# Optimization experiments

Hardware: AMD Instinct MI355X
Metric: run time of the kernel (lower is better)

## Reference

```python
import jax, jax.numpy as jnp
import numpy as np

N_EMBD = 256
N_HEAD = 4
HEAD_DIM = N_EMBD // N_HEAD  # 64


def setup_inputs() -> dict:
    key = jax.random.key(0)
    k_x, k_attn, k_proj = jax.random.split(key, 3)
    B, S = 8, 2048
    x = jax.random.normal(k_x, (B, S, N_EMBD), dtype=jnp.float32)
    # nn.Linear(in, out, bias=False): weight shape [out, in]; y = x @ W.T
    std_attn = 1.0 / np.sqrt(N_EMBD)
    W_attn = jax.random.uniform(k_attn, (3 * N_EMBD, N_EMBD), dtype=jnp.float32,
                                minval=-std_attn, maxval=std_attn)
    W_proj = jax.random.uniform(k_proj, (N_EMBD, N_EMBD), dtype=jnp.float32,
                                minval=-std_attn, maxval=std_attn)
    return {"x": x, "W_attn": W_attn, "W_proj": W_proj}


def reference(x, W_attn, W_proj):
    B, S, C = x.shape
    qkv = jnp.einsum('bsc,oc->bso', x, W_attn)  # [B,S,3C]
    q, k, v = jnp.split(qkv, 3, axis=2)
    # [B,S,C] -> [B,H,S,D]
    def heads(t):
        return t.reshape(B, S, N_HEAD, HEAD_DIM).transpose(0, 2, 1, 3)
    q, k, v = heads(q), heads(k), heads(v)
    scale = 1.0 / np.sqrt(HEAD_DIM)
    scores = jnp.einsum('bhqd,bhkd->bhqk', q, k) * scale  # [B,H,S,S]
    causal = jnp.tril(jnp.ones((S, S), dtype=bool))
    scores = jnp.where(causal, scores, jnp.finfo(scores.dtype).min)
    attn = jax.nn.softmax(scores, axis=-1)
    y = jnp.einsum('bhqk,bhkd->bhqd', attn, v)  # [B,H,S,D]
    y = y.transpose(0, 2, 1, 3).reshape(B, S, C)
    return jnp.einsum('bsc,oc->bso', y, W_proj)
```

## Files before the change

kernel.cpp:

```cpp
#include <hip/hip_runtime.h>
#include <stdint.h>


#define BB 8
#define SS 2048
#define CC 256
#define HH 4
#define DD 64

typedef __attribute__((ext_vector_type(8))) __bf16 bf16x8;
typedef __attribute__((ext_vector_type(4))) __bf16 bf16x4;
typedef __attribute__((ext_vector_type(4))) float f32x4;
typedef __attribute__((ext_vector_type(16))) float f32x16;

#define CM 0.18033688011112042f

static __device__ __forceinline__ uint32_t cvtpk(float lo, float hi) {
  uint32_t r;
  asm("v_cvt_pk_bf16_f32 %0, %1, %2" : "=v"(r) : "v"(lo), "v"(hi));
  return r;
}
static __device__ __forceinline__ void pl32swap(uint32_t& a, uint32_t& b) {
  asm("v_permlane32_swap_b32 %0, %1" : "+v"(a), "+v"(b));
}
union PU { uint32_t u[4]; bf16x8 v; };

static __device__ __forceinline__ int frag_off(int row, int c8) {
  return ((row >> 4) * 8 + (c8 >> 2)) * 512 + (row & 15) * 32 + (c8 & 3) * 8;
}

__global__ __launch_bounds__(256) void cvt3_kernel(const float* __restrict__ x,
                                                   const float* __restrict__ wa,
                                                   const float* __restrict__ wp,
                                                   __bf16* __restrict__ xf,
                                                   __bf16* __restrict__ waf,
                                                   __bf16* __restrict__ wpf) {
  int i = blockIdx.x * blockDim.x + threadIdx.x;
  const float* in; __bf16* out;
  if (i < 524288) {
    in = x + i * 8;
    out = xf + frag_off(i >> 5, i & 31);
  } else if (i < 548864) {
    int j = i - 524288;
    in = wa + j * 8;
    out = waf + frag_off(j >> 5, j & 31);
  } else {
    int k = i - 548864;
    in = wp + k * 8;
    out = wpf + frag_off(k >> 5, k & 31);
  }
  float4 v0 = ((const float4*)in)[0];
  float4 v1 = ((const float4*)in)[1];
  bf16x8 o = { (__bf16)v0.x, (__bf16)v0.y, (__bf16)v0.z, (__bf16)v0.w,
               (__bf16)v1.x, (__bf16)v1.y, (__bf16)v1.z, (__bf16)v1.w };
  *(bf16x8*)out = o;
}

__global__ __launch_bounds__(256) void qkv_gemm(const __bf16* __restrict__ xf,
                                                const __bf16* __restrict__ waf,
                                                __bf16* __restrict__ qf_,
                                                __bf16* __restrict__ kf_,
                                                __bf16* __restrict__ vf_) {
  const int lane = threadIdx.x & 63;
  const int ln = lane & 15, kg = lane >> 4;
  const int w = threadIdx.x >> 6;
  const int xs = blockIdx.x & 7;
  const int j = blockIdx.x >> 3;
  const int otile = j % 12;
  const int rt0 = (xs * 8 + j / 12) * 16 + w * 4;
  const int ot0 = otile * 4;
  const int loff = ln * 32 + kg * 8;
  const bool vmode = (otile >= 8);

  f32x4 acc[4][4] = {};
  for (int cb = 0; cb < 8; ++cb) {
    bf16x8 a[4], wv[4];
#pragma unroll
    for (int i = 0; i < 4; ++i)
      a[i] = *(const bf16x8*)(xf + ((rt0 + i) * 8 + cb) * 512 + loff);
#pragma unroll
    for (int t = 0; t < 4; ++t)
      wv[t] = *(const bf16x8*)(waf + ((ot0 + t) * 8 + cb) * 512 + loff);
    if (vmode) {
#pragma unroll
      for (int i = 0; i < 4; ++i)
#pragma unroll
        for (int t = 0; t < 4; ++t)
          acc[i][t] = __builtin_amdgcn_mfma_f32_16x16x32_bf16(a[i], wv[t], acc[i][t], 0, 0, 0);
    } else {
#pragma unroll
      for (int i = 0; i < 4; ++i)
#pragma unroll
        for (int t = 0; t < 4; ++t)
          acc[i][t] = __builtin_amdgcn_mfma_f32_16x16x32_bf16(wv[t], a[i], acc[i][t], 0, 0, 0);
    }
  }
  const int r0 = rt0 * 16;
  const int o0 = ot0 * 16;
  if (!vmode) {
    const bool isK = (otile >= 4);
    const float sc = isK ? CM : 1.0f;
#pragma unroll
    for (int i = 0; i < 4; ++i) {
      int s = r0 + i * 16 + ln;
      int b = s >> 11, srow = s & 2047;
#pragma unroll
      for (int t = 0; t < 4; ++t) {
        int obase = o0 + t * 16 + kg * 4;
        int oo = obase & 255;
        int h = oo >> 6;
        int bh_off = (b * HH + h) * 131072;
        uint32_t lo = cvtpk(acc[i][t][0] * sc, acc[i][t][1] * sc);
        uint32_t hi2 = cvtpk(acc[i][t][2] * sc, acc[i][t][3] * sc);
        uint2 st = { lo, hi2 };
        if (!isK) {
          int off = bh_off + (srow >> 5) * 2048 + t * 512 + (srow & 31) * 16 + kg * 4;
          *(uint2*)(qf_ + off) = st;
        } else {
          int off = bh_off + (srow >> 6) * 4096 + t * 1024 + (srow & 63) * 16 + kg * 4;
          *(uint2*)(kf_ + off) = st;
        }
      }
    }
  } else {
    const int h = otile - 8;
#pragma unroll
    for (int i = 0; i < 4; ++i) {
      int sg = r0 + i * 16;
      int b = sg >> 11;
      int bh_off = (b * HH + h) * 131072;
      int sbase = (sg & 2047) + kg * 4;
      int off0 = bh_off + (sbase >> 6) * 4096 + ((sbase >> 4) & 3) * 1024 + (sbase & 15);
#pragma unroll
      for (int t = 0; t < 4; ++t) {
        int d = t * 16 + ln;
        uint32_t lo = cvtpk(acc[i][t][0], acc[i][t][1]);
        uint32_t hi2 = cvtpk(acc[i][t][2], acc[i][t][3]);
        uint2 st = { lo, hi2 };
        *(uint2*)(vf_ + off0 + d * 16) = st;
      }
    }
  }
}

__global__ __launch_bounds__(256, 4) void attn_kernel(const __bf16* __restrict__ qf_,
                                                      const __bf16* __restrict__ kf_,
                                                      const __bf16* __restrict__ vf_,
                                                      __bf16* __restrict__ yf) {
  __shared__ float lsum[2][32];
  __shared__ float lacc[2][64][33];
  const int lane = threadIdx.x & 63;
  const int l31 = lane & 31;
  const int hi = lane >> 5;
  const int w = threadIdx.x >> 6;
  const int kh = w & 1;
  const int cp = w >> 1;

  const int bid = blockIdx.x;
  const int xs = bid & 7;
  const int j = bid >> 3;
  const int bh = xs + 8 * (j & 3);
  const int p = j >> 2;
  const int c = (31 - p) * 2 + cp;
  const int q0w = c * 32;

  const int loff = l31 * 16 + hi * 8;
  const int koff = kh * 32;

  const __bf16* Qfb = qf_ + bh * 131072 + c * 2048 + loff;
  const __bf16* Kb  = kf_ + bh * 131072 + loff + kh * 512;
  const __bf16* Vb  = vf_ + bh * 131072 + loff + kh * 2048;

  bf16x8 qf[4];
#pragma unroll
  for (int s = 0; s < 4; ++s) qf[s] = *(const bf16x8*)(Qfb + s * 512);

  const int ntot = (q0w + 95) >> 6;
  const int qrel = l31 + 32 * (c & 1);

  f32x16 acc0 = {}, acc1 = {};
  float lrun = 0.0f;

  for (int kt = 0; kt < ntot; ++kt) {
    bf16x8 ka[4], vfr[2][2];
    {
      const __bf16* Kp = Kb + kt * 4096;
      const __bf16* Vp = Vb + kt * 4096;
#pragma unroll
      for (int s = 0; s < 4; ++s) ka[s] = *(const bf16x8*)(Kp + s * 1024);
      vfr[0][0] = *(const bf16x8*)(Vp);
      vfr[0][1] = *(const bf16x8*)(Vp + 512);
      vfr[1][0] = *(const bf16x8*)(Vp + 1024);
      vfr[1][1] = *(const bf16x8*)(Vp + 1536);
    }

    f32x16 s0 = {};
    __builtin_amdgcn_s_setprio(1);
#pragma unroll
    for (int s = 0; s < 4; ++s) s0 = __builtin_amdgcn_mfma_f32_32x32x16_bf16(ka[s], qf[s], s0, 0, 0, 0);
    __builtin_amdgcn_s_setprio(0);

    if (kt == ntot - 1) {
#pragma unroll
      for (int r = 0; r < 16; ++r) {
        int crow = (r & 3) + 8 * (r >> 2) + 4 * hi;
        s0[r] = (crow + koff <= qrel) ? s0[r] : -1e30f;
      }
    }

#pragma unroll
    for (int r = 0; r < 16; ++r) s0[r] = __builtin_amdgcn_exp2f(s0[r]);

    {
      float sm[8];
#pragma unroll
      for (int r = 0; r < 8; ++r) sm[r] = s0[r] + s0[r + 8];
#pragma unroll
      for (int st = 4; st > 0; st >>= 1)
#pragma unroll
        for (int r = 0; r < 4; ++r) if (r < st) sm[r] += sm[r + st];
      lrun += sm[0];
    }

    bf16x8 pf[2];
#pragma unroll
    for (int g = 0; g < 2; ++g) {
      const int o = g * 8;
      uint32_t a = cvtpk(s0[o + 0], s0[o + 1]);
      uint32_t b = cvtpk(s0[o + 4], s0[o + 5]);
      uint32_t c2 = cvtpk(s0[o + 2], s0[o + 3]);
      uint32_t d2 = cvtpk(s0[o + 6], s0[o + 7]);
      pl32swap(a, b);
      pl32swap(c2, d2);
      PU u; u.u[0] = a; u.u[1] = c2; u.u[2] = b; u.u[3] = d2;
      pf[g] = u.v;
    }

    __builtin_amdgcn_s_setprio(1);
    acc0 = __builtin_amdgcn_mfma_f32_32x32x16_bf16(vfr[0][0], pf[0], acc0, 0, 0, 0);
    acc0 = __builtin_amdgcn_mfma_f32_32x32x16_bf16(vfr[1][0], pf[1], acc0, 0, 0, 0);
    acc1 = __builtin_amdgcn_mfma_f32_32x32x16_bf16(vfr[0][1], pf[0], acc1, 0, 0, 0);
    acc1 = __builtin_amdgcn_mfma_f32_32x32x16_bf16(vfr[1][1], pf[1], acc1, 0, 0, 0);
    __builtin_amdgcn_s_setprio(0);
  }

  lrun += __shfl_xor(lrun, 32);

  if (kh == 1) {
    if (hi == 0) lsum[cp][l31] = lrun;
#pragma unroll
    for (int r = 0; r < 16; ++r) {
      int d0 = (r & 3) + 8 * (r >> 2) + 4 * hi;
      lacc[cp][d0][l31] = acc0[r];
      lacc[cp][32 + d0][l31] = acc1[r];
    }
  }
  __syncthreads();
  if (kh == 0) {
    float L = lrun + lsum[cp][l31];
    float inv = __builtin_amdgcn_rcpf(L);
    const int b = bh >> 2, h = bh & 3;
    __bf16* ytile = yf + (((b * 128 + c * 2 + (l31 >> 4)) * 8 + h * 2) * 512)
                       + (l31 & 15) * 32 + hi * 4;
#pragma unroll
    for (int g = 0; g < 4; ++g) {
      float a0[4], a1[4];
#pragma unroll
      for (int i2 = 0; i2 < 4; ++i2) {
        int d0 = i2 + 8 * g + 4 * hi;
        a0[i2] = (acc0[g * 4 + i2] + lacc[cp][d0][l31]) * inv;
        a1[i2] = (acc1[g * 4 + i2] + lacc[cp][32 + d0][l31]) * inv;
      }
      uint32_t w0 = cvtpk(a0[0], a0[1]);
      uint32_t w1 = cvtpk(a0[2], a0[3]);
      uint2 st0 = { w0, w1 };
      *(uint2*)(ytile + g * 8) = st0;
      w0 = cvtpk(a1[0], a1[1]);
      w1 = cvtpk(a1[2], a1[3]);
      uint2 st1 = { w0, w1 };
      *(uint2*)(ytile + 512 + g * 8) = st1;
    }
  }
}

__global__ __launch_bounds__(256) void proj_gemm(const __bf16* __restrict__ yf,
                                                 const __bf16* __restrict__ wpf,
                                                 float* __restrict__ out) {
  const int lane = threadIdx.x & 63;
  const int ln = lane & 15, kg = lane >> 4;
  const int w = threadIdx.x >> 6;
  const int xs = blockIdx.x & 7;
  const int j = blockIdx.x >> 3;
  const int otile = j & 3;
  const int rt0 = (xs * 8 + (j >> 2)) * 16 + w * 4;
  const int ot0 = otile * 4;
  const int loff = ln * 32 + kg * 8;

  f32x4 acc[4][4] = {};
  for (int cb = 0; cb < 8; ++cb) {
    bf16x8 a[4], wv[4];
#pragma unroll
    for (int i = 0; i < 4; ++i)
      a[i] = *(const bf16x8*)(yf + ((rt0 + i) * 8 + cb) * 512 + loff);
#pragma unroll
    for (int t = 0; t < 4; ++t)
      wv[t] = *(const bf16x8*)(wpf + ((ot0 + t) * 8 + cb) * 512 + loff);
#pragma unroll
    for (int i = 0; i < 4; ++i)
#pragma unroll
      for (int t = 0; t < 4; ++t)
        acc[i][t] = __builtin_amdgcn_mfma_f32_16x16x32_bf16(a[i], wv[t], acc[i][t], 0, 0, 0);
  }
  const int r0 = rt0 * 16;
  const int o0 = ot0 * 16;
#pragma unroll
  for (int i = 0; i < 4; ++i)
#pragma unroll
    for (int t = 0; t < 4; ++t) {
      int o = o0 + t * 16 + ln;
#pragma unroll
      for (int r = 0; r < 4; ++r) {
        int rout = r0 + i * 16 + kg * 4 + r;
        out[rout * 256 + o] = acc[i][t][r];
      }
    }
}

extern "C" void kernel_launch(void* const* d_in, const int* in_sizes, int n_in,
                              void* d_out, int out_size, void* d_ws, size_t ws_size,
                              hipStream_t stream) {
  const float* x = (const float*)d_in[0];
  const float* Wa = (const float*)d_in[1];
  const float* Wp = (const float*)d_in[2];

  char* ws = (char*)d_ws;
  __bf16* xf  = (__bf16*)(ws);
  __bf16* qfb = (__bf16*)(ws + 8388608);
  __bf16* kfb = (__bf16*)(ws + 16777216);
  __bf16* vfb = (__bf16*)(ws + 25165824);
  __bf16* yf  = (__bf16*)(ws + 33554432);
  __bf16* waf = (__bf16*)(ws + 41943040);
  __bf16* wpf = (__bf16*)(ws + 42336256);

  cvt3_kernel<<<2176, 256, 0, stream>>>(x, Wa, Wp, xf, waf, wpf);
  qkv_gemm<<<768, 256, 0, stream>>>(xf, waf, qfb, kfb, vfb);
  attn_kernel<<<1024, 256, 0, stream>>>(qfb, kfb, vfb, yf);
  proj_gemm<<<256, 256, 0, stream>>>(yf, wpf, (float*)d_out);
}
```

Measured before the change: 63.27 us.

## Stage K/V tiles into double-buffered LDS via async global-to-LDS loads

The attention kernel now has the four waves of a block jointly copy each K/V tile into a double-buffered 32 KB LDS area using global_load_lds. The next tile is prefetched while the current one is consumed, and each wave then reads its K/V fragments from LDS instead of global memory. The aim is to remove duplicate global loads, since waves with different query chunks fetch the same K/V, and to hide load latency behind the MFMA work. The cost is a block-wide barrier every iteration and more LDS per block, which may limit occupancy. The reduction scratch reuses the same LDS buffer.

```diff
diff --git a/kernel.cpp b/kernel.cpp
--- a/kernel.cpp
+++ b/kernel.cpp
@@ -147,8 +147,7 @@
                                                       const __bf16* __restrict__ kf_,
                                                       const __bf16* __restrict__ vf_,
                                                       __bf16* __restrict__ yf) {
-  __shared__ float lsum[2][32];
-  __shared__ float lacc[2][64][33];
+  __shared__ char smem[32768];
   const int lane = threadIdx.x & 63;
   const int l31 = lane & 31;
   const int hi = lane >> 5;
@@ -168,8 +167,8 @@
   const int koff = kh * 32;
 
   const __bf16* Qfb = qf_ + bh * 131072 + c * 2048 + loff;
-  const __bf16* Kb  = kf_ + bh * 131072 + loff + kh * 512;
-  const __bf16* Vb  = vf_ + bh * 131072 + loff + kh * 2048;
+  const __bf16* Kt = kf_ + bh * 131072;
+  const __bf16* Vt = vf_ + bh * 131072;
 
   bf16x8 qf[4];
 #pragma unroll
@@ -181,17 +180,38 @@
   f32x16 acc0 = {}, acc1 = {};
   float lrun = 0.0f;
 
+  auto STAGE = [&](int buf, int kt) {
+#pragma unroll
+    for (int ci = 0; ci < 4; ++ci) {
+      int ch = w * 4 + ci;
+      const __bf16* g = (ch < 8 ? Kt + kt * 4096 + ch * 512
+                                : Vt + kt * 4096 + (ch - 8) * 512) + lane * 8;
+      char* l = smem + buf * 16384 + ch * 1024;
+      __builtin_amdgcn_global_load_lds(
+          (const __attribute__((address_space(1))) void*)g,
+          (__attribute__((address_space(3))) void*)l, 16, 0, 0);
+    }
+  };
+
+  STAGE(0, 0);
+  __syncthreads();
+
+  int cur = 0;
   for (int kt = 0; kt < ntot; ++kt) {
+    if (kt + 1 < ntot) STAGE(cur ^ 1, kt + 1);
+
+    const __bf16* kl = (const __bf16*)(smem + cur * 16384);
+    const __bf16* vl = (const __bf16*)(smem + cur * 16384 + 8192);
+
     bf16x8 ka[4], vfr[2][2];
+#pragma unroll
+    for (int s = 0; s < 4; ++s) ka[s] = *(const bf16x8*)(kl + kh * 512 + s * 1024 + loff);
     {
-      const __bf16* Kp = Kb + kt * 4096;
-      const __bf16* Vp = Vb + kt * 4096;
-#pragma unroll
-      for (int s = 0; s < 4; ++s) ka[s] = *(const bf16x8*)(Kp + s * 1024);
-      vfr[0][0] = *(const bf16x8*)(Vp);
-      vfr[0][1] = *(const bf16x8*)(Vp + 512);
-      vfr[1][0] = *(const bf16x8*)(Vp + 1024);
-      vfr[1][1] = *(const bf16x8*)(Vp + 1536);
+      const __bf16* vp = vl + kh * 2048 + loff;
+      vfr[0][0] = *(const bf16x8*)(vp);
+      vfr[0][1] = *(const bf16x8*)(vp + 512);
+      vfr[1][0] = *(const bf16x8*)(vp + 1024);
+      vfr[1][1] = *(const bf16x8*)(vp + 1536);
     }
 
     f32x16 s0 = {};
@@ -242,22 +262,27 @@
     acc1 = __builtin_amdgcn_mfma_f32_32x32x16_bf16(vfr[0][1], pf[0], acc1, 0, 0, 0);
     acc1 = __builtin_amdgcn_mfma_f32_32x32x16_bf16(vfr[1][1], pf[1], acc1, 0, 0, 0);
     __builtin_amdgcn_s_setprio(0);
+
+    __syncthreads();
+    cur ^= 1;
   }
 
   lrun += __shfl_xor(lrun, 32);
 
+  float* lsum = (float*)smem;
+  float* lacc = (float*)(smem + 256);
   if (kh == 1) {
-    if (hi == 0) lsum[cp][l31] = lrun;
+    if (hi == 0) lsum[cp * 32 + l31] = lrun;
 #pragma unroll
     for (int r = 0; r < 16; ++r) {
       int d0 = (r & 3) + 8 * (r >> 2) + 4 * hi;
-      lacc[cp][d0][l31] = acc0[r];
-      lacc[cp][32 + d0][l31] = acc1[r];
+      lacc[(cp * 64 + d0) * 33 + l31] = acc0[r];
+      lacc[(cp * 64 + 32 + d0) * 33 + l31] = acc1[r];
     }
   }
   __syncthreads();
   if (kh == 0) {
-    float L = lrun + lsum[cp][l31];
+    float L = lrun + lsum[cp * 32 + l31];
     float inv = __builtin_amdgcn_rcpf(L);
     const int b = bh >> 2, h = bh & 3;
     __bf16* ytile = yf + (((b * 128 + c * 2 + (l31 >> 4)) * 8 + h * 2) * 512)
@@ -268,8 +293,8 @@
 #pragma unroll
       for (int i2 = 0; i2 < 4; ++i2) {
         int d0 = i2 + 8 * g + 4 * hi;
-        a0[i2] = (acc0[g * 4 + i2] + lacc[cp][d0][l31]) * inv;
-        a1[i2] = (acc1[g * 4 + i2] + lacc[cp][32 + d0][l31]) * inv;
+        a0[i2] = (acc0[g * 4 + i2] + lacc[(cp * 64 + d0) * 33 + l31]) * inv;
+        a1[i2] = (acc1[g * 4 + i2] + lacc[(cp * 64 + 32 + d0) * 33 + l31]) * inv;
       }
       uint32_t w0 = cvtpk(a0[0], a0[1]);
       uint32_t w1 = cvtpk(a0[2], a0[3]);
```

Result: no change. 63.68 us (+0.7%).

## Pair causal query tiles per block for load balance; shrink proj GEMM tiles

Applied to the files above, without the earlier changes.

The attention kernel now launches half as many blocks, and each block handles two query chunks, m and 31-m. This pairing gives every block the same total amount of causal key work and removes the tail imbalance from long and short blocks. Launch bounds drop to 2 blocks per CU, and an extra __syncthreads guards reuse of shared memory between the two phases. Separately, the projection GEMM gives each wave one 16-row tile instead of four and launches four times as many blocks. This raises parallelism but reduces reuse of the weight loads.

```diff
diff --git a/kernel.cpp b/kernel.cpp
--- a/kernel.cpp
+++ b/kernel.cpp
@@ -143,7 +143,7 @@
   }
 }
 
-__global__ __launch_bounds__(256, 4) void attn_kernel(const __bf16* __restrict__ qf_,
+__global__ __launch_bounds__(256, 2) void attn_kernel(const __bf16* __restrict__ qf_,
                                                       const __bf16* __restrict__ kf_,
                                                       const __bf16* __restrict__ vf_,
                                                       __bf16* __restrict__ yf) {
@@ -160,125 +160,134 @@
   const int xs = bid & 7;
   const int j = bid >> 3;
   const int bh = xs + 8 * (j & 3);
-  const int p = j >> 2;
-  const int c = (31 - p) * 2 + cp;
-  const int q0w = c * 32;
+  const int m = j >> 2;
 
   const int loff = l31 * 16 + hi * 8;
   const int koff = kh * 32;
 
-  const __bf16* Qfb = qf_ + bh * 131072 + c * 2048 + loff;
-  const __bf16* Kb  = kf_ + bh * 131072 + loff + kh * 512;
-  const __bf16* Vb  = vf_ + bh * 131072 + loff + kh * 2048;
-
-  bf16x8 qf[4];
-#pragma unroll
-  for (int s = 0; s < 4; ++s) qf[s] = *(const bf16x8*)(Qfb + s * 512);
-
-  const int ntot = (q0w + 95) >> 6;
-  const int qrel = l31 + 32 * (c & 1);
-
-  f32x16 acc0 = {}, acc1 = {};
-  float lrun = 0.0f;
-
-  for (int kt = 0; kt < ntot; ++kt) {
-    bf16x8 ka[4], vfr[2][2];
+  const __bf16* Kb = kf_ + bh * 131072 + loff + kh * 512;
+  const __bf16* Vb = vf_ + bh * 131072 + loff + kh * 2048;
+
+  const int b = bh >> 2, h = bh & 3;
+
+#pragma unroll
+  for (int ph = 0; ph < 2; ++ph) {
+    const int pr = ph ? (31 - m) : m;
+    const int c = 2 * pr + cp;
+    const int q0w = c * 32;
+    const int ntot = pr + 1;
+    const int qrel = l31 + 32 * (c & 1);
+
+    bf16x8 qf[4];
     {
-      const __bf16* Kp = Kb + kt * 4096;
-      const __bf16* Vp = Vb + kt * 4096;
-#pragma unroll
-      for (int s = 0; s < 4; ++s) ka[s] = *(const bf16x8*)(Kp + s * 1024);
-      vfr[0][0] = *(const bf16x8*)(Vp);
-      vfr[0][1] = *(const bf16x8*)(Vp + 512);
-      vfr[1][0] = *(const bf16x8*)(Vp + 1024);
-      vfr[1][1] = *(const bf16x8*)(Vp + 1536);
-    }
-
-    f32x16 s0 = {};
-    __builtin_amdgcn_s_setprio(1);
-#pragma unroll
-    for (int s = 0; s < 4; ++s) s0 = __builtin_amdgcn_mfma_f32_32x32x16_bf16(ka[s], qf[s], s0, 0, 0, 0);
-    __builtin_amdgcn_s_setprio(0);
-
-    if (kt == ntot - 1) {
+      const __bf16* Qfb = qf_ + bh * 131072 + c * 2048 + loff;
+#pragma unroll
+      for (int s = 0; s < 4; ++s) qf[s] = *(const bf16x8*)(Qfb + s * 512);
+    }
+    (void)q0w;
+
+    f32x16 acc0 = {}, acc1 = {};
+    float lrun = 0.0f;
+
+    for (int kt = 0; kt < ntot; ++kt) {
+      bf16x8 ka[4], vfr[2][2];
+      {
+        const __bf16* Kp = Kb + kt * 4096;
+        const __bf16* Vp = Vb + kt * 4096;
+#pragma unroll
+        for (int s = 0; s < 4; ++s) ka[s] = *(const bf16x8*)(Kp + s * 1024);
+        vfr[0][0] = *(const bf16x8*)(Vp);
+        vfr[0][1] = *(const bf16x8*)(Vp + 512);
+        vfr[1][0] = *(const bf16x8*)(Vp + 1024);
+        vfr[1][1] = *(const bf16x8*)(Vp + 1536);
+      }
+
+      f32x16 s0 = {};
+      __builtin_amdgcn_s_setprio(1);
+#pragma unroll
+      for (int s = 0; s < 4; ++s) s0 = __builtin_amdgcn_mfma_f32_32x32x16_bf16(ka[s], qf[s], s0, 0, 0, 0);
+      __builtin_amdgcn_s_setprio(0);
+
+      if (kt == ntot - 1) {
+#pragma unroll
+        for (int r = 0; r < 16; ++r) {
+          int crow = (r & 3) + 8 * (r >> 2) + 4 * hi;
+          s0[r] = (crow + koff <= qrel) ? s0[r] : -1e30f;
+        }
+      }
+
+#pragma unroll
+      for (int r = 0; r < 16; ++r) s0[r] = __builtin_amdgcn_exp2f(s0[r]);
+
+      {
+        float sm[8];
+#pragma unroll
+        for (int r = 0; r < 8; ++r) sm[r] = s0[r] + s0[r + 8];
+#pragma unroll
+        for (int st = 4; st > 0; st >>= 1)
+#pragma unroll
+          for (int r = 0; r < 4; ++r) if (r < st) sm[r] += sm[r + st];
+        lrun += sm[0];
+      }
+
+      bf16x8 pf[2];
+#pragma unroll
+      for (int g = 0; g < 2; ++g) {
+        const int o = g * 8;
+        uint32_t a = cvtpk(s0[o + 0], s0[o + 1]);
+        uint32_t bb2 = cvtpk(s0[o + 4], s0[o + 5]);
+        uint32_t c2 = cvtpk(s0[o + 2], s0[o + 3]);
+        uint32_t d2 = cvtpk(s0[o + 6], s0[o + 7]);
+        pl32swap(a, bb2);
+        pl32swap(c2, d2);
+        PU u; u.u[0] = a; u.u[1] = c2; u.u[2] = bb2; u.u[3] = d2;
+        pf[g] = u.v;
+      }
+
+      __builtin_amdgcn_s_setprio(1);
+      acc0 = __builtin_amdgcn_mfma_f32_32x32x16_bf16(vfr[0][0], pf[0], acc0, 0, 0, 0);
+      acc0 = __builtin_amdgcn_mfma_f32_32x32x16_bf16(vfr[1][0], pf[1], acc0, 0, 0, 0);
+      acc1 = __builtin_amdgcn_mfma_f32_32x32x16_bf16(vfr[0][1], pf[0], acc1, 0, 0, 0);
+      acc1 = __builtin_amdgcn_mfma_f32_32x32x16_bf16(vfr[1][1], pf[1], acc1, 0, 0, 0);
+      __builtin_amdgcn_s_setprio(0);
+    }
+
+    lrun += __shfl_xor(lrun, 32);
+
+    __syncthreads();
+    if (kh == 1) {
+      if (hi == 0) lsum[cp][l31] = lrun;
 #pragma unroll
       for (int r = 0; r < 16; ++r) {
-        int crow = (r & 3) + 8 * (r >> 2) + 4 * hi;
-        s0[r] = (crow + koff <= qrel) ? s0[r] : -1e30f;
-      }
-    }
-
-#pragma unroll
-    for (int r = 0; r < 16; ++r) s0[r] = __builtin_amdgcn_exp2f(s0[r]);
-
-    {
-      float sm[8];
-#pragma unroll
-      for (int r = 0; r < 8; ++r) sm[r] = s0[r] + s0[r + 8];
-#pragma unroll
-      for (int st = 4; st > 0; st >>= 1)
-#pragma unroll
-        for (int r = 0; r < 4; ++r) if (r < st) sm[r] += sm[r + st];
-      lrun += sm[0];
-    }
-
-    bf16x8 pf[2];
-#pragma unroll
-    for (int g = 0; g < 2; ++g) {
-      const int o = g * 8;
-      uint32_t a = cvtpk(s0[o + 0], s0[o + 1]);
-      uint32_t b = cvtpk(s0[o + 4], s0[o + 5]);
-      uint32_t c2 = cvtpk(s0[o + 2], s0[o + 3]);
-      uint32_t d2 = cvtpk(s0[o + 6], s0[o + 7]);
-      pl32swap(a, b);
-      pl32swap(c2, d2);
-      PU u; u.u[0] = a; u.u[1] = c2; u.u[2] = b; u.u[3] = d2;
-      pf[g] = u.v;
-    }
-
-    __builtin_amdgcn_s_setprio(1);
-    acc0 = __builtin_amdgcn_mfma_f32_32x32x16_bf16(vfr[0][0], pf[0], acc0, 0, 0, 0);
-    acc0 = __builtin_amdgcn_mfma_f32_32x32x16_bf16(vfr[1][0], pf[1], acc0, 0, 0, 0);
-    acc1 = __builtin_amdgcn_mfma_f32_32x32x16_bf16(vfr[0][1], pf[0], acc1, 0, 0, 0);
-    acc1 = __builtin_amdgcn_mfma_f32_32x32x16_bf16(vfr[1][1], pf[1], acc1, 0, 0, 0);
-    __builtin_amdgcn_s_setprio(0);
-  }
-
-  lrun += __shfl_xor(lrun, 32);
-
-  if (kh == 1) {
-    if (hi == 0) lsum[cp][l31] = lrun;
-#pragma unroll
-    for (int r = 0; r < 16; ++r) {
-      int d0 = (r & 3) + 8 * (r >> 2) + 4 * hi;
-      lacc[cp][d0][l31] = acc0[r];
-      lacc[cp][32 + d0][l31] = acc1[r];
-    }
-  }
-  __syncthreads();
-  if (kh == 0) {
-    float L = lrun + lsum[cp][l31];
-    float inv = __builtin_amdgcn_rcpf(L);
-    const int b = bh >> 2, h = bh & 3;
-    __bf16* ytile = yf + (((b * 128 + c * 2 + (l31 >> 4)) * 8 + h * 2) * 512)
-                       + (l31 & 15) * 32 + hi * 4;
-#pragma unroll
-    for (int g = 0; g < 4; ++g) {
-      float a0[4], a1[4];
-#pragma unroll
-      for (int i2 = 0; i2 < 4; ++i2) {
-        int d0 = i2 + 8 * g + 4 * hi;
-        a0[i2] = (acc0[g * 4 + i2] + lacc[cp][d0][l31]) * inv;
-        a1[i2] = (acc1[g * 4 + i2] + lacc[cp][32 + d0][l31]) * inv;
-      }
-      uint32_t w0 = cvtpk(a0[0], a0[1]);
-      uint32_t w1 = cvtpk(a0[2], a0[3]);
-      uint2 st0 = { w0, w1 };
-      *(uint2*)(ytile + g * 8) = st0;
-      w0 = cvtpk(a1[0], a1[1]);
-      w1 = cvtpk(a1[2], a1[3]);
-      uint2 st1 = { w0, w1 };
-      *(uint2*)(ytile + 512 + g * 8) = st1;
+        int d0 = (r & 3) + 8 * (r >> 2) + 4 * hi;
+        lacc[cp][d0][l31] = acc0[r];
+        lacc[cp][32 + d0][l31] = acc1[r];
+      }
+    }
+    __syncthreads();
+    if (kh == 0) {
+      float L = lrun + lsum[cp][l31];
+      float inv = __builtin_amdgcn_rcpf(L);
+      __bf16* ytile = yf + (((b * 128 + c * 2 + (l31 >> 4)) * 8 + h * 2) * 512)
+                         + (l31 & 15) * 32 + hi * 4;
+#pragma unroll
+      for (int g = 0; g < 4; ++g) {
+        float a0[4], a1[4];
+#pragma unroll
+        for (int i2 = 0; i2 < 4; ++i2) {
+          int d0 = i2 + 8 * g + 4 * hi;
+          a0[i2] = (acc0[g * 4 + i2] + lacc[cp][d0][l31]) * inv;
+          a1[i2] = (acc1[g * 4 + i2] + lacc[cp][32 + d0][l31]) * inv;
+        }
+        uint32_t w0 = cvtpk(a0[0], a0[1]);
+        uint32_t w1 = cvtpk(a0[2], a0[3]);
+        uint2 st0 = { w0, w1 };
+        *(uint2*)(ytile + g * 8) = st0;
+        w0 = cvtpk(a1[0], a1[1]);
+        w1 = cvtpk(a1[2], a1[3]);
+        uint2 st1 = { w0, w1 };
+        *(uint2*)(ytile + 512 + g * 8) = st1;
+      }
     }
   }
 }
@@ -292,38 +301,32 @@
   const int xs = blockIdx.x & 7;
   const int j = blockIdx.x >> 3;
   const int otile = j & 3;
-  const int rt0 = (xs * 8 + (j >> 2)) * 16 + w * 4;
+  const int rt0 = (xs * 32 + (j >> 2)) * 4 + w;
   const int ot0 = otile * 4;
   const int loff = ln * 32 + kg * 8;
 
-  f32x4 acc[4][4] = {};
+  f32x4 acc[4] = {};
   for (int cb = 0; cb < 8; ++cb) {
-    bf16x8 a[4], wv[4];
-#pragma unroll
-    for (int i = 0; i < 4; ++i)
-      a[i] = *(const bf16x8*)(yf + ((rt0 + i) * 8 + cb) * 512 + loff);
+    bf16x8 a, wv[4];
+    a = *(const bf16x8*)(yf + (rt0 * 8 + cb) * 512 + loff);
 #pragma unroll
     for (int t = 0; t < 4; ++t)
       wv[t] = *(const bf16x8*)(wpf + ((ot0 + t) * 8 + cb) * 512 + loff);
 #pragma unroll
-    for (int i = 0; i < 4; ++i)
-#pragma unroll
-      for (int t = 0; t < 4; ++t)
-        acc[i][t] = __builtin_amdgcn_mfma_f32_16x16x32_bf16(a[i], wv[t], acc[i][t], 0, 0, 0);
+    for (int t = 0; t < 4; ++t)
+      acc[t] = __builtin_amdgcn_mfma_f32_16x16x32_bf16(a, wv[t], acc[t], 0, 0, 0);
   }
   const int r0 = rt0 * 16;
   const int o0 = ot0 * 16;
 #pragma unroll
-  for (int i = 0; i < 4; ++i)
-#pragma unroll
-    for (int t = 0; t < 4; ++t) {
-      int o = o0 + t * 16 + ln;
-#pragma unroll
-      for (int r = 0; r < 4; ++r) {
-        int rout = r0 + i * 16 + kg * 4 + r;
-        out[rout * 256 + o] = acc[i][t][r];
-      }
-    }
+  for (int t = 0; t < 4; ++t) {
+    int o = o0 + t * 16 + ln;
+#pragma unroll
+    for (int r = 0; r < 4; ++r) {
+      int rout = r0 + kg * 4 + r;
+      out[rout * 256 + o] = acc[t][r];
+    }
+  }
 }
 
 extern "C" void kernel_launch(void* const* d_in, const int* in_sizes, int n_in,
@@ -344,6 +347,6 @@
 
   cvt3_kernel<<<2176, 256, 0, stream>>>(x, Wa, Wp, xf, waf, wpf);
   qkv_gemm<<<768, 256, 0, stream>>>(xf, waf, qfb, kfb, vfb);
-  attn_kernel<<<1024, 256, 0, stream>>>(qfb, kfb, vfb, yf);
-  proj_gemm<<<256, 256, 0, stream>>>(yf, wpf, (float*)d_out);
-}
+  attn_kernel<<<512, 256, 0, stream>>>(qfb, kfb, vfb, yf);
+  proj_gemm<<<1024, 256, 0, stream>>>(yf, wpf, (float*)d_out);
+}
```

Result: slower. 65.06 us (+2.8%).

## Fuse x fp32-to-bf16 conversion into QKV GEMM via LDS staging; shrink proj tiles

Applied to the files above, without the earlier changes.

The separate conversion of x to bf16 fragment layout is removed. The QKV GEMM now loads fp32 x directly, converts it, and stages it through double-buffered shared memory that all four waves share, which saves the write and re-read of an 8 MB intermediate. The projection GEMM uses one row tile per wave instead of four and launches four times as many blocks to improve occupancy. The costs are redundant fp32 reads of x across the 12 output-tile blocks per row group and a barrier per k-step.

```diff
diff --git a/kernel.cpp b/kernel.cpp
--- a/kernel.cpp
+++ b/kernel.cpp
@@ -29,55 +29,76 @@
   return ((row >> 4) * 8 + (c8 >> 2)) * 512 + (row & 15) * 32 + (c8 & 3) * 8;
 }
 
-__global__ __launch_bounds__(256) void cvt3_kernel(const float* __restrict__ x,
-                                                   const float* __restrict__ wa,
+__global__ __launch_bounds__(256) void cvtw_kernel(const float* __restrict__ wa,
                                                    const float* __restrict__ wp,
-                                                   __bf16* __restrict__ xf,
                                                    __bf16* __restrict__ waf,
                                                    __bf16* __restrict__ wpf) {
-  int i = blockIdx.x * blockDim.x + threadIdx.x;
+  int i = blockIdx.x * 256 + threadIdx.x;
   const float* in; __bf16* out;
-  if (i < 524288) {
-    in = x + i * 8;
-    out = xf + frag_off(i >> 5, i & 31);
-  } else if (i < 548864) {
-    int j = i - 524288;
-    in = wa + j * 8;
-    out = waf + frag_off(j >> 5, j & 31);
+  if (i < 24576) {
+    in = wa + i * 8;
+    out = waf + frag_off(i >> 5, i & 31);
   } else {
-    int k = i - 548864;
+    int k = i - 24576;
     in = wp + k * 8;
     out = wpf + frag_off(k >> 5, k & 31);
   }
   float4 v0 = ((const float4*)in)[0];
   float4 v1 = ((const float4*)in)[1];
-  bf16x8 o = { (__bf16)v0.x, (__bf16)v0.y, (__bf16)v0.z, (__bf16)v0.w,
-               (__bf16)v1.x, (__bf16)v1.y, (__bf16)v1.z, (__bf16)v1.w };
-  *(bf16x8*)out = o;
-}
-
-__global__ __launch_bounds__(256) void qkv_gemm(const __bf16* __restrict__ xf,
+  PU u;
+  u.u[0] = cvtpk(v0.x, v0.y);
+  u.u[1] = cvtpk(v0.z, v0.w);
+  u.u[2] = cvtpk(v1.x, v1.y);
+  u.u[3] = cvtpk(v1.z, v1.w);
+  *(bf16x8*)out = u.v;
+}
+
+__global__ __launch_bounds__(256) void qkv_gemm(const float* __restrict__ x,
                                                 const __bf16* __restrict__ waf,
                                                 __bf16* __restrict__ qf_,
                                                 __bf16* __restrict__ kf_,
                                                 __bf16* __restrict__ vf_) {
-  const int lane = threadIdx.x & 63;
+  __shared__ __bf16 xls[2][8192];
+  const int tid = threadIdx.x;
+  const int lane = tid & 63;
   const int ln = lane & 15, kg = lane >> 4;
-  const int w = threadIdx.x >> 6;
+  const int w = tid >> 6;
   const int xs = blockIdx.x & 7;
   const int j = blockIdx.x >> 3;
   const int otile = j % 12;
-  const int rt0 = (xs * 8 + j / 12) * 16 + w * 4;
+  const int rg = xs * 8 + j / 12;
+  const int r0b = rg * 256;
   const int ot0 = otile * 4;
   const int loff = ln * 32 + kg * 8;
   const bool vmode = (otile >= 8);
 
+  auto STAGE = [&](int buf, int cb) {
+#pragma unroll
+    for (int ii = 0; ii < 4; ++ii) {
+      int q = ii * 256 + tid;
+      int tile = q >> 6, rr = (q >> 2) & 15, c8i = q & 3;
+      const float* p = x + (r0b + tile * 16 + rr) * 256 + cb * 32 + c8i * 8;
+      float4 v0 = *(const float4*)p;
+      float4 v1 = *(const float4*)(p + 4);
+      PU u;
+      u.u[0] = cvtpk(v0.x, v0.y);
+      u.u[1] = cvtpk(v0.z, v0.w);
+      u.u[2] = cvtpk(v1.x, v1.y);
+      u.u[3] = cvtpk(v1.z, v1.w);
+      *(bf16x8*)&xls[buf][q * 8] = u.v;
+    }
+  };
+
   f32x4 acc[4][4] = {};
+  STAGE(0, 0);
+  int cur = 0;
   for (int cb = 0; cb < 8; ++cb) {
+    __syncthreads();
+    if (cb + 1 < 8) STAGE(cur ^ 1, cb + 1);
     bf16x8 a[4], wv[4];
 #pragma unroll
     for (int i = 0; i < 4; ++i)
-      a[i] = *(const bf16x8*)(xf + ((rt0 + i) * 8 + cb) * 512 + loff);
+      a[i] = *(const bf16x8*)&xls[cur][(w * 4 + i) * 512 + loff];
 #pragma unroll
     for (int t = 0; t < 4; ++t)
       wv[t] = *(const bf16x8*)(waf + ((ot0 + t) * 8 + cb) * 512 + loff);
@@ -94,8 +115,10 @@
         for (int t = 0; t < 4; ++t)
           acc[i][t] = __builtin_amdgcn_mfma_f32_16x16x32_bf16(wv[t], a[i], acc[i][t], 0, 0, 0);
     }
-  }
-  const int r0 = rt0 * 16;
+    cur ^= 1;
+  }
+
+  const int r0 = r0b + w * 64;
   const int o0 = ot0 * 16;
   if (!vmode) {
     const bool isK = (otile >= 4);
@@ -292,38 +315,32 @@
   const int xs = blockIdx.x & 7;
   const int j = blockIdx.x >> 3;
   const int otile = j & 3;
-  const int rt0 = (xs * 8 + (j >> 2)) * 16 + w * 4;
+  const int rt0 = (xs * 32 + (j >> 2)) * 4 + w;
   const int ot0 = otile * 4;
   const int loff = ln * 32 + kg * 8;
 
-  f32x4 acc[4][4] = {};
+  f32x4 acc[4] = {};
   for (int cb = 0; cb < 8; ++cb) {
-    bf16x8 a[4], wv[4];
-#pragma unroll
-    for (int i = 0; i < 4; ++i)
-      a[i] = *(const bf16x8*)(yf + ((rt0 + i) * 8 + cb) * 512 + loff);
+    bf16x8 a, wv[4];
+    a = *(const bf16x8*)(yf + (rt0 * 8 + cb) * 512 + loff);
 #pragma unroll
     for (int t = 0; t < 4; ++t)
       wv[t] = *(const bf16x8*)(wpf + ((ot0 + t) * 8 + cb) * 512 + loff);
 #pragma unroll
-    for (int i = 0; i < 4; ++i)
-#pragma unroll
-      for (int t = 0; t < 4; ++t)
-        acc[i][t] = __builtin_amdgcn_mfma_f32_16x16x32_bf16(a[i], wv[t], acc[i][t], 0, 0, 0);
+    for (int t = 0; t < 4; ++t)
+      acc[t] = __builtin_amdgcn_mfma_f32_16x16x32_bf16(a, wv[t], acc[t], 0, 0, 0);
   }
   const int r0 = rt0 * 16;
   const int o0 = ot0 * 16;
 #pragma unroll
-  for (int i = 0; i < 4; ++i)
-#pragma unroll
-    for (int t = 0; t < 4; ++t) {
-      int o = o0 + t * 16 + ln;
-#pragma unroll
-      for (int r = 0; r < 4; ++r) {
-        int rout = r0 + i * 16 + kg * 4 + r;
-        out[rout * 256 + o] = acc[i][t][r];
-      }
-    }
+  for (int t = 0; t < 4; ++t) {
+    int o = o0 + t * 16 + ln;
+#pragma unroll
+    for (int r = 0; r < 4; ++r) {
+      int rout = r0 + kg * 4 + r;
+      out[rout * 256 + o] = acc[t][r];
+    }
+  }
 }
 
 extern "C" void kernel_launch(void* const* d_in, const int* in_sizes, int n_in,
@@ -334,16 +351,15 @@
   const float* Wp = (const float*)d_in[2];
 
   char* ws = (char*)d_ws;
-  __bf16* xf  = (__bf16*)(ws);
-  __bf16* qfb = (__bf16*)(ws + 8388608);
-  __bf16* kfb = (__bf16*)(ws + 16777216);
-  __bf16* vfb = (__bf16*)(ws + 25165824);
-  __bf16* yf  = (__bf16*)(ws + 33554432);
-  __bf16* waf = (__bf16*)(ws + 41943040);
-  __bf16* wpf = (__bf16*)(ws + 42336256);
-
-  cvt3_kernel<<<2176, 256, 0, stream>>>(x, Wa, Wp, xf, waf, wpf);
-  qkv_gemm<<<768, 256, 0, stream>>>(xf, waf, qfb, kfb, vfb);
+  __bf16* qfb = (__bf16*)(ws);
+  __bf16* kfb = (__bf16*)(ws + 8388608);
+  __bf16* vfb = (__bf16*)(ws + 16777216);
+  __bf16* yf  = (__bf16*)(ws + 25165824);
+  __bf16* waf = (__bf16*)(ws + 33554432);
+  __bf16* wpf = (__bf16*)(ws + 33947648);
+
+  cvtw_kernel<<<128, 256, 0, stream>>>(Wa, Wp, waf, wpf);
+  qkv_gemm<<<768, 256, 0, stream>>>(x, waf, qfb, kfb, vfb);
   attn_kernel<<<1024, 256, 0, stream>>>(qfb, kfb, vfb, yf);
-  proj_gemm<<<256, 256, 0, stream>>>(yf, wpf, (float*)d_out);
-}
+  proj_gemm<<<1024, 256, 0, stream>>>(yf, wpf, (float*)d_out);
+}
```

Measured after the change: 70.91 us. 1.12x slower.
